# Optimization experiments

Hardware: AMD Instinct MI355X
Metric: run time of the kernel (lower is better)

Reference implementation:

```python
import jax, jax.numpy as jnp
import numpy as np
from jax import lax

BITS_P = 8   # parameter fake-quant bits
BITS_A = 8   # activation fake-quant bits
D_STATE = 16
DT_RANK = 2
EPS = 1e-5


def fake_quant(t, bits):
    """Min-max fake quantization (forward math of QuantizationFunction)."""
    mn, mx = t.min(), t.max()
    step = (mx - mn) / (2 ** bits - 1)
    step_safe = jnp.where(step == 0, 1.0, step)
    q = jnp.round((jnp.clip(t, mn, mx) - mn) / step_safe) * step_safe + mn
    return jnp.where(step == 0, t, q)


def quant_ste(t, bits):
    # straight-through estimator (backward returns grad unchanged)
    return t + lax.stop_gradient(fake_quant(t, bits) - t)


def layernorm(x, g, b):
    mu = x.mean(-1, keepdims=True)
    var = ((x - mu) ** 2).mean(-1, keepdims=True)
    return (x - mu) * lax.rsqrt(var + EPS) * g + b


def mamba_block(x4d, ln_g, ln_b, W_in, conv_w, conv_b, W_xproj, W_dt, dt_bias, A_log, D_ssm, W_out):
    B, M, H, W = x4d.shape
    L = H * W
    di = W_in.shape[1] // 2  # d_inner = 2*M
    seq = x4d.reshape(B, M, L).transpose(0, 2, 1)          # [B,L,M]
    h = layernorm(seq, ln_g, ln_b)
    xz = h @ W_in                                           # [B,L,2*di]
    xs, z = xz[..., :di], xz[..., di:]
    # causal depthwise conv1d, kernel 4
    xc = xs.transpose(0, 2, 1)                              # [B,di,L]
    xc = lax.conv_general_dilated(xc, conv_w[:, None, :], (1,), ((3, 0),),
                                  dimension_numbers=('NCH', 'OIH', 'NCH'),
                                  feature_group_count=di)
    xc = jax.nn.silu(xc + conv_b[None, :, None]).transpose(0, 2, 1)  # [B,L,di]
    dbl = xc @ W_xproj                                      # [B,L,dt_rank+2*ds]
    dt_r = dbl[..., :DT_RANK]
    Bm = dbl[..., DT_RANK:DT_RANK + D_STATE]                # [B,L,ds]
    Cm = dbl[..., DT_RANK + D_STATE:]                       # [B,L,ds]
    dt = jax.nn.softplus(dt_r @ W_dt + dt_bias)             # [B,L,di]
    A = -jnp.exp(A_log)                                     # [di,ds]

    def step(hprev, inp):
        dt_t, B_t, C_t, x_t = inp                           # [B,di],[B,ds],[B,ds],[B,di]
        dA = jnp.exp(dt_t[..., None] * A)                   # [B,di,ds]
        hn = hprev * dA + (dt_t * x_t)[..., None] * B_t[:, None, :]
        y = jnp.einsum('bds,bs->bd', hn, C_t)
        return hn, y

    h0 = jnp.zeros((B, di, D_STATE), x4d.dtype)
    _, ys = lax.scan(step, h0, (dt.transpose(1, 0, 2), Bm.transpose(1, 0, 2),
                                Cm.transpose(1, 0, 2), xc.transpose(1, 0, 2)))
    ys = ys.transpose(1, 0, 2)                              # [B,L,di]
    ys = (ys + xc * D_ssm) * jax.nn.silu(z)
    out = ys @ W_out                                        # [B,L,M]
    seq = seq + out                                         # residual
    return seq.transpose(0, 2, 1).reshape(B, M, H, W)


def reference(x, stem_w, bn_gamma, bn_beta, bn_mean, bn_var,
              ln_g, ln_b, W_in, conv_w, conv_b, W_xproj, W_dt, dt_bias,
              A_log, D_ssm, W_out, proj_w, fc_w, fc_b):
    B = x.shape[0]
    # stem: fake-quant conv -> BN (eval stats) -> SiLU
    w_q = quant_ste(stem_w, BITS_P)
    h = lax.conv_general_dilated(x, w_q, (2, 2), ((1, 1), (1, 1)),
                                 dimension_numbers=('NCHW', 'OIHW', 'NCHW'))
    h = (h - bn_mean[None, :, None, None]) * lax.rsqrt(bn_var + EPS)[None, :, None, None]
    h = h * bn_gamma[None, :, None, None] + bn_beta[None, :, None, None]
    h = jax.nn.silu(h)                                      # [B,32,16,16]
    for i in range(ln_g.shape[0]):
        h = mamba_block(h, ln_g[i], ln_b[i], W_in[i], conv_w[i], conv_b[i],
                        W_xproj[i], W_dt[i], dt_bias[i], A_log[i], D_ssm[i], W_out[i])
    # fake-quant 1x1 conv head + fc
    pw = quant_ste(proj_w, BITS_P)
    h = lax.conv_general_dilated(h, pw, (1, 1), ((0, 0), (0, 0)),
                                 dimension_numbers=('NCHW', 'OIHW', 'NCHW'))
    h = h.reshape(B, -1)                                    # [B,2048]
    fw = quant_ste(fc_w, BITS_P)
    h = h @ fw.T + fc_b                                     # [B,512]
    h = jax.nn.sigmoid(h)
    return quant_ste(h, BITS_A)


def setup_inputs() -> dict:
    key = jax.random.key(0)
    ks = jax.random.split(key, 20)
    B, M, di, nl = 2048, 32, 64, 2
    s = 0.05
    inp = {
        'x': jax.random.normal(ks[0], (B, 2, 32, 32), jnp.float32),
        'stem_w': jax.random.normal(ks[1], (M, 2, 3, 3), jnp.float32) * 0.2,
        'bn_gamma': jnp.ones((M,), jnp.float32),
        'bn_beta': jnp.zeros((M,), jnp.float32),
        'bn_mean': jax.random.normal(ks[2], (M,), jnp.float32) * 0.1,
        'bn_var': jax.random.uniform(ks[3], (M,), jnp.float32, 0.5, 1.5),
        'ln_g': jnp.ones((nl, M), jnp.float32),
        'ln_b': jnp.zeros((nl, M), jnp.float32),
        'W_in': jax.random.normal(ks[4], (nl, M, 2 * di), jnp.float32) * s,
        'conv_w': jax.random.normal(ks[5], (nl, di, 4), jnp.float32) * 0.2,
        'conv_b': jnp.zeros((nl, di), jnp.float32),
        'W_xproj': jax.random.normal(ks[6], (nl, di, DT_RANK + 2 * D_STATE), jnp.float32) * s,
        'W_dt': jax.random.normal(ks[7], (nl, DT_RANK, di), jnp.float32) * s,
        'dt_bias': jax.random.normal(ks[8], (nl, di), jnp.float32) * 0.1,
        'A_log': jnp.log(jnp.tile(jnp.arange(1.0, D_STATE + 1.0), (nl, di, 1))).astype(jnp.float32),
        'D_ssm': jnp.ones((nl, di), jnp.float32),
        'W_out': jax.random.normal(ks[9], (nl, di, M), jnp.float32) * s,
        'proj_w': jax.random.normal(ks[10], (8, M, 1, 1), jnp.float32) * 0.1,
        'fc_w': jax.random.normal(ks[11], (512, 8 * 16 * 16), jnp.float32) * 0.02,
        'fc_b': jnp.zeros((512,), jnp.float32),
    }
    return inp
```

## Files before the change

### kernel.cpp

```cpp
#include <hip/hip_runtime.h>
#include <hip/hip_fp16.h>
#include <math.h>

#define NB   2048
#define M_   32
#define L_   256
#define DI   64
#define DS_  16
#define EPSF 1e-5f

__device__ __forceinline__ float sigmf(float x){ return 1.0f/(1.0f+__expf(-x)); }
__device__ __forceinline__ float siluf(float x){ return x*sigmf(x); }

__device__ __forceinline__ void blk_minmax(float& mn, float& mx){
  for (int off = 32; off >= 1; off >>= 1){
    mn = fminf(mn, __shfl_down(mn, off, 64));
    mx = fmaxf(mx, __shfl_down(mx, off, 64));
  }
  __shared__ float smn[4], smx[4];
  int w = threadIdx.x >> 6;
  if ((threadIdx.x & 63) == 0){ smn[w] = mn; smx[w] = mx; }
  __syncthreads();
  if (threadIdx.x == 0){
    int nw = (int)(blockDim.x >> 6);
    for (int i = 1; i < nw; ++i){ mn = fminf(mn, smn[i]); mx = fmaxf(mx, smx[i]); }
  }
}

__global__ void k_minmax_part(const float* __restrict__ t, int n, float* __restrict__ part){
  float mn = 3.402823466e38f, mx = -3.402823466e38f;
  for (int i = blockIdx.x*blockDim.x + threadIdx.x; i < n; i += gridDim.x*blockDim.x){
    float v = t[i]; mn = fminf(mn, v); mx = fmaxf(mx, v);
  }
  blk_minmax(mn, mx);
  if (threadIdx.x == 0){ part[blockIdx.x*2] = mn; part[blockIdx.x*2+1] = mx; }
}

__global__ void k_minmax_final(const float* __restrict__ part, int nparts, float* __restrict__ qp){
  float mn = 3.402823466e38f, mx = -3.402823466e38f;
  for (int i = threadIdx.x; i < nparts; i += blockDim.x){
    mn = fminf(mn, part[i*2]); mx = fmaxf(mx, part[i*2+1]);
  }
  blk_minmax(mn, mx);
  if (threadIdx.x == 0){
    qp[0] = mn; qp[1] = mx; qp[2] = (mx - mn) / 255.0f;
  }
}

__global__ void k_quant(const float* __restrict__ t, float* __restrict__ q, int n,
                        const float* __restrict__ qp){
  float mn = qp[0], mx = qp[1], step = qp[2];
  bool zero = (step == 0.0f);
  for (int i = blockIdx.x*blockDim.x + threadIdx.x; i < n; i += gridDim.x*blockDim.x){
    float v = t[i];
    float c = fminf(fmaxf(v, mn), mx);
    float r = rintf((c - mn) / (zero ? 1.0f : step));
    float o = fmaf(r, step, mn);
    q[i] = zero ? v : o;
  }
}

__launch_bounds__(256)
__global__ void k_stem(const float* __restrict__ x, const float* __restrict__ wq,
                       const float* __restrict__ bn_g, const float* __restrict__ bn_b,
                       const float* __restrict__ bn_m, const float* __restrict__ bn_v,
                       __half* __restrict__ h){
  int b = blockIdx.x;
  __shared__ float xs[2048];
  const float* xb = x + (size_t)b*2048;
  for (int i = threadIdx.x; i < 2048; i += 256) xs[i] = xb[i];
  __syncthreads();
  int l = threadIdx.x;
  int oy = l >> 4, ox = l & 15;
  for (int m = 0; m < M_; ++m){
    float acc = 0.f;
    #pragma unroll
    for (int c = 0; c < 2; ++c){
      #pragma unroll
      for (int ky = 0; ky < 3; ++ky){
        int iy = oy*2 - 1 + ky;
        if (iy < 0 || iy >= 32) continue;
        #pragma unroll
        for (int kx = 0; kx < 3; ++kx){
          int ix = ox*2 - 1 + kx;
          if (ix < 0 || ix >= 32) continue;
          acc = fmaf(xs[c*1024 + iy*32 + ix], wq[((m*2 + c)*3 + ky)*3 + kx], acc);
        }
      }
    }
    float r = (acc - bn_m[m]) * rsqrtf(bn_v[m] + EPSF) * bn_g[m] + bn_b[m];
    h[((size_t)b*M_ + m)*L_ + l] = __float2half(siluf(r));
  }
}

__launch_bounds__(256)
__global__ void k_ab(const __half* __restrict__ h, const float* __restrict__ lng,
                     const float* __restrict__ lnb, const float* __restrict__ W_in,
                     const float* __restrict__ conv_w, const float* __restrict__ conv_b,
                     const float* __restrict__ W_xproj,
                     __half* __restrict__ xc, __half* __restrict__ bc){
  const int b = blockIdx.x, l = threadIdx.x;
  __shared__ __half2 xsb[L_][33];
  __shared__ __half2 xcb[L_][33];
  const __half* hb = h + (size_t)b*M_*L_;
  float hnreg[M_];
  {
    float s = 0.f;
    #pragma unroll
    for (int m = 0; m < M_; ++m){ hnreg[m] = __half2float(hb[m*L_ + l]); s += hnreg[m]; }
    float mu = s * (1.0f/32.0f);
    float v = 0.f;
    #pragma unroll
    for (int m = 0; m < M_; ++m){ float dd = hnreg[m]-mu; v += dd*dd; }
    float rs = rsqrtf(v*(1.0f/32.0f) + EPSF);
    #pragma unroll
    for (int m = 0; m < M_; ++m) hnreg[m] = (hnreg[m]-mu)*rs*lng[m] + lnb[m];
  }
  #pragma unroll
  for (int p = 0; p < 4; ++p){
    float acc[16];
    #pragma unroll
    for (int j = 0; j < 16; ++j) acc[j] = 0.f;
    #pragma unroll
    for (int m = 0; m < M_; ++m){
      float hv = hnreg[m];
      const float* wr = W_in + m*128 + p*16;
      #pragma unroll
      for (int j = 0; j < 16; ++j) acc[j] = fmaf(hv, wr[j], acc[j]);
    }
    #pragma unroll
    for (int q = 0; q < 8; ++q)
      xsb[l][p*8 + q] = __floats2half2_rn(acc[2*q], acc[2*q+1]);
  }
  __syncthreads();
  {
    const int r3 = l-3, r2 = l-2, r1 = l-1;
    #pragma unroll
    for (int q = 0; q < 32; ++q){
      float2 a0 = (r3 >= 0) ? __half22float2(xsb[r3][q]) : make_float2(0.f,0.f);
      float2 a1 = (r2 >= 0) ? __half22float2(xsb[r2][q]) : make_float2(0.f,0.f);
      float2 a2 = (r1 >= 0) ? __half22float2(xsb[r1][q]) : make_float2(0.f,0.f);
      float2 a3 = __half22float2(xsb[l][q]);
      int d0 = 2*q, d1 = 2*q+1;
      float s0 = fmaf(conv_w[d0*4+0],a0.x, fmaf(conv_w[d0*4+1],a1.x,
                 fmaf(conv_w[d0*4+2],a2.x, fmaf(conv_w[d0*4+3],a3.x, conv_b[d0]))));
      float s1 = fmaf(conv_w[d1*4+0],a0.y, fmaf(conv_w[d1*4+1],a1.y,
                 fmaf(conv_w[d1*4+2],a2.y, fmaf(conv_w[d1*4+3],a3.y, conv_b[d1]))));
      xcb[l][q] = __floats2half2_rn(siluf(s0), siluf(s1));
    }
  }
  __syncthreads();
  {
    float4* xg = (float4*)(xc + (size_t)b*L_*DI);
    #pragma unroll
    for (int k = 0; k < 8; ++k){
      int g = k*256 + l;
      int row = g >> 3, f4 = g & 7;
      float4 v;
      __half2* vh = (__half2*)&v;
      vh[0] = xcb[row][f4*4+0];
      vh[1] = xcb[row][f4*4+1];
      vh[2] = xcb[row][f4*4+2];
      vh[3] = xcb[row][f4*4+3];
      xg[g] = v;
    }
  }
  float acc[34];
  {
    #pragma unroll
    for (int j = 0; j < 34; ++j) acc[j] = 0.f;
    #pragma unroll
    for (int q = 0; q < 32; ++q){
      float2 xv = __half22float2(xcb[l][q]);
      const float* w0 = W_xproj + (2*q)*34;
      const float* w1 = w0 + 34;
      #pragma unroll
      for (int j = 0; j < 34; ++j)
        acc[j] = fmaf(xv.x, w0[j], fmaf(xv.y, w1[j], acc[j]));
    }
  }
  __syncthreads();
  #pragma unroll
  for (int q = 0; q < 8; ++q) xcb[l][q]   = __floats2half2_rn(acc[2+2*q],  acc[3+2*q]);
  #pragma unroll
  for (int q = 0; q < 8; ++q) xcb[l][8+q] = __floats2half2_rn(acc[18+2*q], acc[19+2*q]);
  xcb[l][16] = __floats2half2_rn(acc[0], acc[1]);
  __syncthreads();
  {
    __half2* bg = (__half2*)(bc + (size_t)b*L_*40);
    #pragma unroll
    for (int k = 0; k < 17; ++k){
      int g = k*256 + l;
      int row = g / 17, c = g - row*17;
      bg[row*20 + c] = xcb[row][c];
    }
  }
}

__attribute__((amdgpu_waves_per_eu(1)))
__launch_bounds__(64)
__global__ void k_scan(__half* __restrict__ xc, const __half* __restrict__ bc,
                       const float* __restrict__ W_dt, const float* __restrict__ dt_bias,
                       const float* __restrict__ A_log, const float* __restrict__ D_ssm){
  const int b = blockIdx.x, d = threadIdx.x;
  __shared__ float4 bcs4[320];
  __shared__ float4 xcs4[512];
  const __half* bcsh = (const __half*)bcs4;
  const __half* xcs  = (const __half*)xcs4;
  const float LOG2E = 1.44269504088896340736f;
  const float wdt0 = W_dt[d], wdt1 = W_dt[64+d], dtb = dt_bias[d], Dd = D_ssm[d];
  float hst[DS_];
  #pragma unroll
  for (int s = 0; s < DS_; ++s) hst[s] = 0.f;
  const float a0 = -__expf(A_log[d*DS_]) * LOG2E;
  bool ok = true;
  #pragma unroll
  for (int s = 1; s < DS_; ++s){
    float as = -__expf(A_log[d*DS_ + s]) * LOG2E;
    ok = ok && (fabsf(as - (float)(s+1)*a0) <= 1e-4f*fabsf(as));
  }
  const bool fast = (__all((int)ok) != 0);
  if (fast){
    const float4* gb = (const float4*)(bc + (size_t)b*L_*40);
    const float4* gx = (const float4*)(xc + (size_t)b*L_*DI);
    __half* xout = xc + (size_t)b*L_*DI + d;
    for (int c = 0; c < 4; ++c){
      __syncthreads();
      #pragma unroll
      for (int k = 0; k < 5; ++k) bcs4[k*64 + d] = gb[c*320 + k*64 + d];
      #pragma unroll
      for (int k = 0; k < 8; ++k) xcs4[k*64 + d] = gx[c*512 + k*64 + d];
      __syncthreads();
      __half2 Bc[8], Cc[8], dt2;
      __half  xvh;
      {
        const __half2* r0 = (const __half2*)bcsh;
        #pragma unroll
        for (int s2 = 0; s2 < 8; ++s2){ Bc[s2] = r0[s2]; Cc[s2] = r0[8+s2]; }
        dt2 = r0[16];
        xvh = xcs[d];
      }
      for (int i = 0; i < 64; ++i){
        const int ip = (i < 63) ? i+1 : i;
        const __half2* rn = (const __half2*)(bcsh + ip*40);
        __half2 nB[8], nC[8];
        #pragma unroll
        for (int s2 = 0; s2 < 8; ++s2){ nB[s2] = rn[s2]; nC[s2] = rn[8+s2]; }
        __half2 ndt = rn[16];
        __half  nxv = xcs[ip*DI + d];
        float2 dtp = __half22float2(dt2);
        float tt = fmaf(dtp.x, wdt0, fmaf(dtp.y, wdt1, dtb));
        float e  = __expf(-fabsf(tt));
        float dtv = fmaxf(tt, 0.f) + __logf(1.f + e);
        float xv = __half2float(xvh);
        float dtx = dtv * xv;
        float r1 = exp2f(dtv * a0);
        float r2 = r1*r1, r3 = r2*r1, r4 = r2*r2;
        float r5 = r4*r1, r6 = r4*r2, r7 = r4*r3, r8 = r4*r4;
        float dA[16] = {r1,r2,r3,r4,r5,r6,r7,r8,
                        r8*r1,r8*r2,r8*r3,r8*r4,r8*r5,r8*r6,r8*r7,r8*r8};
        float yp = 0.f;
        #pragma unroll
        for (int s2 = 0; s2 < 8; ++s2){
          float2 Bp = __half22float2(Bc[s2]);
          float2 Cp = __half22float2(Cc[s2]);
          hst[2*s2]   = fmaf(hst[2*s2],   dA[2*s2],   dtx*Bp.x);
          yp = fmaf(hst[2*s2],   Cp.x, yp);
          hst[2*s2+1] = fmaf(hst[2*s2+1], dA[2*s2+1], dtx*Bp.y);
          yp = fmaf(hst[2*s2+1], Cp.y, yp);
        }
        xout[(size_t)(c*64 + i)*DI] = __float2half(fmaf(xv, Dd, yp));
        #pragma unroll
        for (int s2 = 0; s2 < 8; ++s2){ Bc[s2] = nB[s2]; Cc[s2] = nC[s2]; }
        dt2 = ndt; xvh = nxv;
      }
    }
  } else {
    float A2r[DS_];
    #pragma unroll
    for (int s = 0; s < DS_; ++s) A2r[s] = -__expf(A_log[d*DS_ + s]) * LOG2E;
    const __half* rowg = bc + (size_t)b*L_*40;
    __half* xpg = xc + (size_t)b*L_*DI + d;
    for (int ll = 0; ll < L_; ++ll){
      float xv = __half2float(*xpg);
      float t0 = __half2float(rowg[32]), t1 = __half2float(rowg[33]);
      float tt = fmaf(t0, wdt0, fmaf(t1, wdt1, dtb));
      float e  = __expf(-fabsf(tt));
      float dtv = fmaxf(tt, 0.f) + __logf(1.f + e);
      float dtx = dtv * xv;
      float yp = 0.f;
      #pragma unroll
      for (int s = 0; s < DS_; ++s){
        float dA = exp2f(dtv * A2r[s]);
        hst[s] = fmaf(hst[s], dA, dtx * __half2float(rowg[s]));
        yp = fmaf(hst[s], __half2float(rowg[16+s]), yp);
      }
      *xpg = __float2half(fmaf(xv, Dd, yp));
      rowg += 40; xpg += DI;
    }
  }
}

__launch_bounds__(256, 3)
__global__ void k_c(const __half* __restrict__ xc, const float* __restrict__ lng,
                    const float* __restrict__ lnb, const float* __restrict__ W_in,
                    const float* __restrict__ W_out, __half* __restrict__ h){
  const int b = blockIdx.x, l = threadIdx.x;
  __half* hb = h + (size_t)b*M_*L_;
  float hnreg[M_], hraw[M_];
  {
    float s = 0.f;
    #pragma unroll
    for (int m = 0; m < M_; ++m){ hraw[m] = __half2float(hb[m*L_ + l]); s += hraw[m]; }
    float mu = s * (1.0f/32.0f);
    float v = 0.f;
    #pragma unroll
    for (int m = 0; m < M_; ++m){ float dd = hraw[m]-mu; v += dd*dd; }
    float rs = rsqrtf(v*(1.0f/32.0f) + EPSF);
    #pragma unroll
    for (int m = 0; m < M_; ++m) hnreg[m] = (hraw[m]-mu)*rs*lng[m] + lnb[m];
  }
  const __half2* yrow = (const __half2*)(xc + ((size_t)b*L_ + l)*DI);
  float accm[M_];
  #pragma unroll
  for (int m = 0; m < M_; ++m) accm[m] = 0.f;
  #pragma unroll
  for (int c2 = 0; c2 < 2; ++c2){
    float z[32];
    #pragma unroll
    for (int j = 0; j < 32; ++j) z[j] = 0.f;
    #pragma unroll
    for (int m = 0; m < M_; ++m){
      float hv = hnreg[m];
      const float* wr = W_in + m*128 + 64 + c2*32;
      #pragma unroll
      for (int j = 0; j < 32; ++j) z[j] = fmaf(hv, wr[j], z[j]);
    }
    #pragma unroll
    for (int j2 = 0; j2 < 16; ++j2){
      float2 yv = __half22float2(yrow[c2*16 + j2]);
      float g0 = yv.x * siluf(z[2*j2]);
      float g1 = yv.y * siluf(z[2*j2+1]);
      const float* w0 = W_out + (c2*32 + 2*j2)*32;
      const float* w1 = w0 + 32;
      #pragma unroll
      for (int m = 0; m < M_; ++m)
        accm[m] = fmaf(g0, w0[m], fmaf(g1, w1[m], accm[m]));
    }
  }
  #pragma unroll
  for (int m = 0; m < M_; ++m)
    hb[m*L_ + l] = __float2half(hraw[m] + accm[m]);
}

__launch_bounds__(256)
__global__ void k_proj(const __half* __restrict__ h, const float* __restrict__ pw,
                       float* __restrict__ h2){
  int b = blockIdx.x;
  __shared__ float hsd[M_*L_];
  for (int i = threadIdx.x; i < M_*L_; i += 256)
    hsd[i] = __half2float(h[(size_t)b*M_*L_ + i]);
  __syncthreads();
  int l = threadIdx.x;
  #pragma unroll
  for (int c = 0; c < 8; ++c){
    float acc = 0.f;
    #pragma unroll
    for (int m = 0; m < M_; ++m) acc = fmaf(hsd[m*L_ + l], pw[c*M_ + m], acc);
    h2[(size_t)b*2048 + c*L_ + l] = acc;
  }
}

__launch_bounds__(256)
__global__ void k_fc(const float* __restrict__ A, const float* __restrict__ W,
                     const float* __restrict__ bias, float* __restrict__ out){
  int bi = blockIdx.x, bj = blockIdx.y;
  __shared__ float As[32][68];
  __shared__ float Ws[32][68];
  int tid = threadIdx.x;
  int ti = tid >> 4, tj = tid & 15;
  float acc[4][4];
  #pragma unroll
  for (int u=0;u<4;++u){
    #pragma unroll
    for (int v=0;v<4;++v) acc[u][v]=0.f;
  }
  for (int k0 = 0; k0 < 2048; k0 += 32){
    __syncthreads();
    #pragma unroll
    for (int r8 = 0; r8 < 8; ++r8){
      int i = tid + r8*256;
      int r = i >> 5, c = i & 31;
      As[c][r] = A[(size_t)(bi*64+r)*2048 + k0 + c];
      Ws[c][r] = W[(size_t)(bj*64+r)*2048 + k0 + c];
    }
    __syncthreads();
    #pragma unroll
    for (int k = 0; k < 32; ++k){
      float4 av = *(const float4*)&As[k][ti*4];
      float4 wv = *(const float4*)&Ws[k][tj*4];
      float a4[4] = {av.x,av.y,av.z,av.w};
      float w4[4] = {wv.x,wv.y,wv.z,wv.w};
      #pragma unroll
      for (int u=0;u<4;++u){
        #pragma unroll
        for (int v=0;v<4;++v) acc[u][v] = fmaf(a4[u], w4[v], acc[u][v]);
      }
    }
  }
  #pragma unroll
  for (int u=0;u<4;++u){
    int r = bi*64 + ti*4 + u;
    #pragma unroll
    for (int v=0;v<4;++v){
      int c = bj*64 + tj*4 + v;
      out[(size_t)r*512 + c] = sigmf(acc[u][v] + bias[c]);
    }
  }
}

static const size_t OF_H    = 0;
static const size_t OF_XC   = 8388608;
static const size_t OF_BC   = 25165824;
static const size_t OF_H2   = 35651584;
static const size_t OF_LG   = 39845888;
static const size_t OF_WQF  = 40894464;
static const size_t OF_WQS  = 41943040;
static const size_t OF_WQP  = 41944064;
static const size_t OF_PART = 41944576;
static const size_t OF_QP   = 41945088;
static const size_t WS_FLOATS_NEEDED = 41945104;

extern "C" void kernel_launch(void* const* d_in, const int* in_sizes, int n_in,
                              void* d_out, int out_size, void* d_ws, size_t ws_size,
                              hipStream_t stream){
  (void)in_sizes; (void)n_in; (void)out_size;
  if (ws_size < WS_FLOATS_NEEDED * sizeof(float)) return;
  const float* x      = (const float*)d_in[0];
  const float* stem_w = (const float*)d_in[1];
  const float* bn_g   = (const float*)d_in[2];
  const float* bn_b   = (const float*)d_in[3];
  const float* bn_m   = (const float*)d_in[4];
  const float* bn_v   = (const float*)d_in[5];
  const float* ln_g   = (const float*)d_in[6];
  const float* ln_b   = (const float*)d_in[7];
  const float* W_in   = (const float*)d_in[8];
  const float* conv_w = (const float*)d_in[9];
  const float* conv_b = (const float*)d_in[10];
  const float* W_xp   = (const float*)d_in[11];
  const float* W_dt   = (const float*)d_in[12];
  const float* dt_b   = (const float*)d_in[13];
  const float* A_log  = (const float*)d_in[14];
  const float* D_ssm  = (const float*)d_in[15];
  const float* W_out  = (const float*)d_in[16];
  const float* proj_w = (const float*)d_in[17];
  const float* fc_w   = (const float*)d_in[18];
  const float* fc_b   = (const float*)d_in[19];
  float* ws   = (float*)d_ws;
  __half* bh  = (__half*)(ws + OF_H);
  __half* bxc = (__half*)(ws + OF_XC);
  __half* bbc = (__half*)(ws + OF_BC);
  float* bh2  = ws + OF_H2;
  float* blg  = ws + OF_LG;
  float* wqf  = ws + OF_WQF;
  float* wqs  = ws + OF_WQS;
  float* wqp  = ws + OF_WQP;
  float* part = ws + OF_PART;
  float* qp   = ws + OF_QP;

  k_minmax_part<<<1,256,0,stream>>>(stem_w, 576, part);
  k_minmax_final<<<1,256,0,stream>>>(part, 1, qp+0);
  k_quant<<<3,256,0,stream>>>(stem_w, wqs, 576, qp+0);

  k_minmax_part<<<1,256,0,stream>>>(proj_w, 256, part);
  k_minmax_final<<<1,256,0,stream>>>(part, 1, qp+4);
  k_quant<<<1,256,0,stream>>>(proj_w, wqp, 256, qp+4);

  k_minmax_part<<<256,256,0,stream>>>(fc_w, 1048576, part);
  k_minmax_final<<<1,256,0,stream>>>(part, 256, qp+8);
  k_quant<<<1024,256,0,stream>>>(fc_w, wqf, 1048576, qp+8);

  k_stem<<<NB,256,0,stream>>>(x, wqs, bn_g, bn_b, bn_m, bn_v, bh);

  for (int i = 0; i < 2; ++i){
    k_ab<<<NB,256,0,stream>>>(bh, ln_g+i*32, ln_b+i*32, W_in+i*4096,
                              conv_w+i*256, conv_b+i*64, W_xp+i*2176, bxc, bbc);
    k_scan<<<NB,64,0,stream>>>(bxc, bbc, W_dt+i*128, dt_b+i*64,
                               A_log+i*1024, D_ssm+i*64);
    k_c<<<NB,256,0,stream>>>(bxc, ln_g+i*32, ln_b+i*32, W_in+i*4096,
                             W_out+i*2048, bh);
  }

  k_proj<<<NB,256,0,stream>>>(bh, wqp, bh2);
  dim3 fcg(32, 8);
  k_fc<<<fcg,256,0,stream>>>(bh2, wqf, fc_b, blg);

  k_minmax_part<<<256,256,0,stream>>>(blg, 1048576, part);
  k_minmax_final<<<1,256,0,stream>>>(part, 256, qp+12);
  k_quant<<<1024,256,0,stream>>>(blg, (float*)d_out, 1048576, qp+12);
}
```

Baseline: 993.2 us.

## Pack four batch scans per block and drop barriers and register prefetch

The SSM scan kernel now runs four independent batch items per 256-thread block, one wavefront each, with per-wave shared-memory staging buffers. The block-wide barriers around staging are removed because each wave only touches its own buffers. The explicit register double-buffering of the next row's B/C/dt/x is replaced by direct LDS reads each step. The waves_per_eu(1) hint is dropped. The aim is better CU occupancy and less barrier overhead, at the cost of more LDS per block and exposed LDS latency in the serial loop. It also relies on lockstep execution within a wave for correctness.

Measured after the change: 905.0 us. 1.1x faster.

```diff
diff --git a/kernel.cpp b/kernel.cpp
--- a/kernel.cpp
+++ b/kernel.cpp
@@ -197,14 +197,16 @@
   }
 }
 
-__attribute__((amdgpu_waves_per_eu(1)))
-__launch_bounds__(64)
+__launch_bounds__(256)
 __global__ void k_scan(__half* __restrict__ xc, const __half* __restrict__ bc,
                        const float* __restrict__ W_dt, const float* __restrict__ dt_bias,
                        const float* __restrict__ A_log, const float* __restrict__ D_ssm){
-  const int b = blockIdx.x, d = threadIdx.x;
-  __shared__ float4 bcs4[320];
-  __shared__ float4 xcs4[512];
+  const int w = threadIdx.x >> 6, d = threadIdx.x & 63;
+  const int b = blockIdx.x*4 + w;
+  __shared__ float4 bcs4_all[4][320];
+  __shared__ float4 xcs4_all[4][512];
+  float4* bcs4 = bcs4_all[w];
+  float4* xcs4 = xcs4_all[w];
   const __half* bcsh = (const __half*)bcs4;
   const __half* xcs  = (const __half*)xcs4;
   const float LOG2E = 1.44269504088896340736f;
@@ -225,34 +227,17 @@
     const float4* gx = (const float4*)(xc + (size_t)b*L_*DI);
     __half* xout = xc + (size_t)b*L_*DI + d;
     for (int c = 0; c < 4; ++c){
-      __syncthreads();
       #pragma unroll
       for (int k = 0; k < 5; ++k) bcs4[k*64 + d] = gb[c*320 + k*64 + d];
       #pragma unroll
       for (int k = 0; k < 8; ++k) xcs4[k*64 + d] = gx[c*512 + k*64 + d];
-      __syncthreads();
-      __half2 Bc[8], Cc[8], dt2;
-      __half  xvh;
-      {
-        const __half2* r0 = (const __half2*)bcsh;
-        #pragma unroll
-        for (int s2 = 0; s2 < 8; ++s2){ Bc[s2] = r0[s2]; Cc[s2] = r0[8+s2]; }
-        dt2 = r0[16];
-        xvh = xcs[d];
-      }
       for (int i = 0; i < 64; ++i){
-        const int ip = (i < 63) ? i+1 : i;
-        const __half2* rn = (const __half2*)(bcsh + ip*40);
-        __half2 nB[8], nC[8];
-        #pragma unroll
-        for (int s2 = 0; s2 < 8; ++s2){ nB[s2] = rn[s2]; nC[s2] = rn[8+s2]; }
-        __half2 ndt = rn[16];
-        __half  nxv = xcs[ip*DI + d];
-        float2 dtp = __half22float2(dt2);
+        const __half2* row2 = (const __half2*)(bcsh + i*40);
+        float2 dtp = __half22float2(row2[16]);
         float tt = fmaf(dtp.x, wdt0, fmaf(dtp.y, wdt1, dtb));
         float e  = __expf(-fabsf(tt));
         float dtv = fmaxf(tt, 0.f) + __logf(1.f + e);
-        float xv = __half2float(xvh);
+        float xv = __half2float(xcs[i*DI + d]);
         float dtx = dtv * xv;
         float r1 = exp2f(dtv * a0);
         float r2 = r1*r1, r3 = r2*r1, r4 = r2*r2;
@@ -262,17 +247,14 @@
         float yp = 0.f;
         #pragma unroll
         for (int s2 = 0; s2 < 8; ++s2){
-          float2 Bp = __half22float2(Bc[s2]);
-          float2 Cp = __half22float2(Cc[s2]);
+          float2 Bp = __half22float2(row2[s2]);
+          float2 Cp = __half22float2(row2[8+s2]);
           hst[2*s2]   = fmaf(hst[2*s2],   dA[2*s2],   dtx*Bp.x);
           yp = fmaf(hst[2*s2],   Cp.x, yp);
           hst[2*s2+1] = fmaf(hst[2*s2+1], dA[2*s2+1], dtx*Bp.y);
           yp = fmaf(hst[2*s2+1], Cp.y, yp);
         }
         xout[(size_t)(c*64 + i)*DI] = __float2half(fmaf(xv, Dd, yp));
-        #pragma unroll
-        for (int s2 = 0; s2 < 8; ++s2){ Bc[s2] = nB[s2]; Cc[s2] = nC[s2]; }
-        dt2 = ndt; xvh = nxv;
       }
     }
   } else {
@@ -485,8 +467,8 @@
   for (int i = 0; i < 2; ++i){
     k_ab<<<NB,256,0,stream>>>(bh, ln_g+i*32, ln_b+i*32, W_in+i*4096,
                               conv_w+i*256, conv_b+i*64, W_xp+i*2176, bxc, bbc);
-    k_scan<<<NB,64,0,stream>>>(bxc, bbc, W_dt+i*128, dt_b+i*64,
-                               A_log+i*1024, D_ssm+i*64);
+    k_scan<<<NB/4,256,0,stream>>>(bxc, bbc, W_dt+i*128, dt_b+i*64,
+                                  A_log+i*1024, D_ssm+i*64);
     k_c<<<NB,256,0,stream>>>(bxc, ln_g+i*32, ln_b+i*32, W_in+i*4096,
                              W_out+i*2048, bh);
   }
```
